# Kernel tuning notes

Hardware: AMD Instinct MI355X
Metric: run time of the kernel (lower is better)

## Reference

```python
import jax, jax.numpy as jnp
import numpy as np

N_EXPERT_CAPACITY = 2  # init kwarg; k = S * capacity // E


def setup_inputs() -> dict:
    key = jax.random.key(0)
    k1, k2, k3, k4 = jax.random.split(key, 4)
    B, S, D, E, F = 8, 1024, 1024, 8, 2048
    # kaiming-uniform-ish scales
    x = jax.random.normal(k1, (B, S, D), dtype=jnp.float32)
    choice_w = jax.random.uniform(k2, (E, D), dtype=jnp.float32, minval=-1.0, maxval=1.0) * (1.0 / np.sqrt(D))
    w1 = jax.random.uniform(k3, (E, D, F), dtype=jnp.float32, minval=-1.0, maxval=1.0) * (1.0 / np.sqrt(D))
    w2 = jax.random.uniform(k4, (E, F, D), dtype=jnp.float32, minval=-1.0, maxval=1.0) * (1.0 / np.sqrt(F))
    return {"x": x, "choice_w": choice_w, "w1": w1, "w2": w2}


def reference(x, choice_w, w1, w2):
    B, S, D = x.shape
    E = choice_w.shape[0]
    k = S * N_EXPERT_CAPACITY // E  # tokens per expert (expert-choice)
    # router softmax over experts: [B, S, E]
    probs = jax.nn.softmax(jnp.einsum('bsd,ed->bse', x, choice_w), axis=-1)
    # each expert picks its top-k tokens: G, I are [B, E, k]
    G, I = jax.lax.top_k(jnp.swapaxes(probs, -1, -2), k)
    # dispatch: gather tokens instead of one-hot matmul (same math)
    x_in = jnp.take_along_axis(x[:, None, :, :], I[..., None], axis=2)  # [B, E, k, D]
    # per-expert MLP with SiLU
    h = jax.nn.silu(jnp.einsum('bekd,edf->bekf', x_in, w1))  # [B, E, k, F]
    x_mlp = jnp.einsum('bekf,efd->bekd', h, w2)              # [B, E, k, D]
    # combine: weighted scatter-add back to token positions (equals P,G,x_mlp einsum)
    b_idx = jnp.arange(B)[:, None, None]  # [B,1,1] broadcasts with I [B,E,k]
    out = jnp.zeros_like(x).at[b_idx, I].add(G[..., None] * x_mlp)
    return out
```

## Files before the change

### kernel.cpp

```cpp
#include <hip/hip_runtime.h>
#include <hip/hip_bf16.h>
#include <math.h>

#define B_   8
#define S_   1024
#define D_   1024
#define E_   8
#define F_   2048
#define KCAP 256

typedef __bf16 bf16x8 __attribute__((ext_vector_type(8)));
typedef float  floatx4 __attribute__((ext_vector_type(4)));
typedef unsigned short ushortx8 __attribute__((ext_vector_type(8)));

__device__ __forceinline__ unsigned short f2b(float f) {
    union { float f; unsigned int u; } v; v.f = f;
    unsigned int u = v.u;
    u += 0x7fffu + ((u >> 16) & 1u);
    return (unsigned short)(u >> 16);
}
__device__ __forceinline__ float b2f(unsigned short u) {
    union { unsigned int u; float f; } v; v.u = ((unsigned)u) << 16; return v.f;
}

__device__ __forceinline__ void gl_lds16(const void* g, void* l) {
    __builtin_amdgcn_global_load_lds(
        (const __attribute__((address_space(1))) void*)g,
        (__attribute__((address_space(3))) void*)l, 16, 0, 0);
}

__device__ __forceinline__ unsigned long long topk_key(float p, int s) {
    return (((unsigned long long)__float_as_uint(p)) << 10) | (unsigned)(S_ - 1 - s);
}

#define PREP_DECODE(T, INP, OUTP, RV, CV, C0, R0) do { \
    int t_ = (T); \
    if (t_ < 4096) { \
        int e_ = t_ >> 9, tt_ = t_ & 511; \
        INP = w1 + (size_t)e_ * D_ * F_;  OUTP = w1t + (size_t)e_ * D_ * F_; \
        RV = D_; CV = F_; C0 = (tt_ & 63) * 32; R0 = (tt_ >> 6) * 128; \
    } else { \
        int t2_ = t_ - 4096; \
        int e_ = t2_ >> 9, tt_ = t2_ & 511; \
        INP = w2 + (size_t)e_ * D_ * F_;  OUTP = w2t + (size_t)e_ * D_ * F_; \
        RV = F_; CV = D_; C0 = (tt_ & 31) * 32; R0 = (tt_ >> 5) * 128; \
    } \
} while (0)

__device__ __forceinline__ void transpose_persist(
    const float* __restrict__ w1, const float* __restrict__ w2,
    unsigned short* __restrict__ w1t, unsigned short* __restrict__ w2t,
    float (*tile)[128][33], int T0, int Tend, int stride, int tid)
{
    const int lrow = tid >> 3;
    const int seg  = tid & 7;
    const int c    = tid >> 3;
    const int k    = tid & 7;

    const float* inp; unsigned short* outp; int R, C, c0, r0;
    PREP_DECODE(T0, inp, outp, R, C, c0, r0);
    float4 v[4];
#pragma unroll
    for (int i = 0; i < 4; i++)
        v[i] = *(const float4*)(inp + (size_t)(r0 + lrow + i * 32) * C + c0 + seg * 4);

    int buf = 0;
    for (int T = T0; T < Tend; T += stride) {
        unsigned short* oute = outp;
        const int Rr = R, cc0 = c0, rr0 = r0;
#pragma unroll
        for (int i = 0; i < 4; i++) {
            const int rr = lrow + i * 32;
            tile[buf][rr][seg * 4 + 0] = v[i].x;
            tile[buf][rr][seg * 4 + 1] = v[i].y;
            tile[buf][rr][seg * 4 + 2] = v[i].z;
            tile[buf][rr][seg * 4 + 3] = v[i].w;
        }
        if (T + stride < Tend) {
            PREP_DECODE(T + stride, inp, outp, R, C, c0, r0);
#pragma unroll
            for (int i = 0; i < 4; i++)
                v[i] = *(const float4*)(inp + (size_t)(r0 + lrow + i * 32) * C + c0 + seg * 4);
        }
        __builtin_amdgcn_sched_barrier(0);
        asm volatile("s_waitcnt lgkmcnt(0)" ::: "memory");
        __builtin_amdgcn_s_barrier();
        __builtin_amdgcn_sched_barrier(0);
#pragma unroll
        for (int srep = 0; srep < 2; srep++) {
            const int s8 = k + srep * 8;
            ushortx8 o;
#pragma unroll
            for (int j = 0; j < 8; j++) o[j] = f2b(tile[buf][s8 * 8 + j][c]);
            *(ushortx8*)(oute + (size_t)(cc0 + c) * Rr + rr0 + s8 * 8) = o;
        }
        buf ^= 1;
    }
}

__global__ void router_w1t_kernel(const float* __restrict__ x, const float* __restrict__ cw,
                                  float* __restrict__ probs, unsigned short* __restrict__ xb,
                                  const float* __restrict__ w1, const float* __restrict__ w2,
                                  unsigned short* __restrict__ w1t, unsigned short* __restrict__ w2t) {
    const int bid = blockIdx.x;
    const int tid = threadIdx.x;
    __shared__ float tile[2][128][33];

    if (bid < 384) {
        transpose_persist(w1, w2, w1t, w2t, tile, bid, 4096, 384, tid);
        return;
    }

    int gid  = (bid - 384) * 256 + tid;
    int wave = gid >> 6;
    int lane = gid & 63;
    int b = wave >> 10;
    int s = wave & (S_ - 1);
    const float* xrow = x + ((size_t)b * S_ + s) * D_;
    unsigned short* xbrow = xb + ((size_t)b * S_ + s) * D_;
    float acc[E_];
#pragma unroll
    for (int e = 0; e < E_; e++) acc[e] = 0.f;
#pragma unroll
    for (int it = 0; it < D_ / 256; it++) {
        int i = it * 256 + lane * 4;
        float4 xv = *(const float4*)(xrow + i);
        ushort4 o;
        o.x = f2b(xv.x); o.y = f2b(xv.y); o.z = f2b(xv.z); o.w = f2b(xv.w);
        *(ushort4*)(xbrow + i) = o;
#pragma unroll
        for (int e = 0; e < E_; e++) {
            float4 wv = *(const float4*)(cw + e * D_ + i);
            acc[e] = fmaf(xv.x, wv.x, fmaf(xv.y, wv.y, fmaf(xv.z, wv.z, fmaf(xv.w, wv.w, acc[e]))));
        }
    }
#pragma unroll
    for (int e = 0; e < E_; e++) {
        float v = acc[e];
#pragma unroll
        for (int off = 32; off >= 1; off >>= 1) v += __shfl_down(v, off, 64);
        acc[e] = v;
    }
    if (lane == 0) {
        float m = acc[0];
#pragma unroll
        for (int e = 1; e < E_; e++) m = fmaxf(m, acc[e]);
        float sum = 0.f;
#pragma unroll
        for (int e = 0; e < E_; e++) { acc[e] = __expf(acc[e] - m); sum += acc[e]; }
        float inv = 1.f / sum;
#pragma unroll
        for (int e = 0; e < E_; e++) probs[((size_t)b * E_ + e) * S_ + s] = acc[e] * inv;
    }
}

__global__ void topk_kernel(const float* __restrict__ probs, int* __restrict__ I,
                            float* __restrict__ G, unsigned short* __restrict__ Pmap) {
    const int be = blockIdx.x;
    const int b = be >> 3, e = be & 7;
    const int tid = threadIdx.x;
    __shared__ unsigned long long keys[S_];
    const float* rowp = probs + (size_t)be * S_;
#pragma unroll
    for (int q = 0; q < 4; q++) {
        const int s = q * 256 + tid;
        keys[s] = topk_key(rowp[s], s);
        Pmap[((size_t)(b * S_ + s)) * E_ + e] = 0;
    }
    __syncthreads();
    unsigned long long my[4];
    int r[4] = {0, 0, 0, 0};
#pragma unroll
    for (int q = 0; q < 4; q++) my[q] = keys[q * 256 + tid];
#pragma unroll 8
    for (int t = 0; t < S_; t++) {
        const unsigned long long kt = keys[t];
#pragma unroll
        for (int q = 0; q < 4; q++) r[q] += (kt > my[q]);
    }
#pragma unroll
    for (int q = 0; q < 4; q++) {
        if (r[q] < KCAP) {
            const int s = q * 256 + tid;
            I[be * KCAP + r[q]] = s;
            G[be * KCAP + r[q]] = rowp[s];
            Pmap[((size_t)(b * S_ + s)) * E_ + e] = (unsigned short)(r[q] + 1);
        }
    }
}


union GemmTransSm {
    struct {
        unsigned short Asm[128 * 64];
        unsigned short Bsm[128 * 64];
        unsigned int   ArowS[128];
    } g;
    float tile[2][128][33];
};

__global__ __launch_bounds__(256, 4) void gemm1_w2t_kernel(
    const unsigned short* __restrict__ xb,
    const unsigned short* __restrict__ w1t_,
    const int* __restrict__ I,
    unsigned short* __restrict__ H,
    const float* __restrict__ w1, const float* __restrict__ w2,
    unsigned short* __restrict__ w1t, unsigned short* __restrict__ w2t)
{
    __shared__ __align__(16) GemmTransSm sm;
    const int g   = blockIdx.x;
    const int tid = threadIdx.x;

    if (g >= 2048) {
        transpose_persist(w1, w2, w1t, w2t, sm.tile, 4096 + (g - 2048), 8192, 384, tid);
        return;
    }

    const int e  = g & 7;
    const int rr = g >> 3;
    const int b  = rr >> 5;
    const int t5 = rr & 31;
    const int be = b * 8 + e;
    const int mt = t5 & 1;
    const int nt = t5 >> 1;

    if (tid < 128) {
        int tok = I[(size_t)be * KCAP + mt * 128 + tid];
        sm.g.ArowS[tid] = (unsigned)((b * S_ + tok) * D_);
    }
    __syncthreads();

    const int r8   = tid >> 3;
    const int kseg = (tid & 7) ^ (r8 & 7);
    unsigned aoffW[4];
#pragma unroll
    for (int w = 0; w < 4; w++) aoffW[w] = sm.g.ArowS[w * 32 + r8] + kseg * 8;
    const size_t boff0 = ((size_t)e * F_ + nt * 128 + r8) * D_ + kseg * 8;

    const int lane = tid & 63;
    const int wv   = tid >> 6;
    const int wm   = (wv & 1) * 64;
    const int wn   = (wv >> 1) * 64;
    const int l15  = lane & 15;
    const int quad = lane >> 4;
    const int x0   = (quad ^ (l15 & 7)) * 8;

    int aoffs[4], boffs[4];
#pragma unroll
    for (int i = 0; i < 4; i++) {
        aoffs[i] = (wm + i * 16 + l15) * 64 + x0;
        boffs[i] = (wn + i * 16 + l15) * 64 + x0;
    }

    floatx4 acc[4][4];
#pragma unroll
    for (int i = 0; i < 4; i++)
#pragma unroll
        for (int j = 0; j < 4; j++) acc[i][j] = (floatx4){0.f, 0.f, 0.f, 0.f};

    for (int k0 = 0; k0 < D_; k0 += 64) {
#pragma unroll
        for (int w = 0; w < 4; w++) {
            gl_lds16(xb   + aoffW[w] + k0,                    &sm.g.Asm[(w * 256 + tid) * 8]);
            gl_lds16(w1t_ + boff0 + (size_t)w * 32 * D_ + k0, &sm.g.Bsm[(w * 256 + tid) * 8]);
        }
        __syncthreads();
        bf16x8 af[4], bfr[4];
#pragma unroll
        for (int i = 0; i < 4; i++) {
            af[i]  = *(const bf16x8*)&sm.g.Asm[aoffs[i]];
            bfr[i] = *(const bf16x8*)&sm.g.Bsm[boffs[i]];
        }
#pragma unroll
        for (int i = 0; i < 4; i++)
#pragma unroll
            for (int j = 0; j < 4; j++)
                acc[i][j] = __builtin_amdgcn_mfma_f32_16x16x32_bf16(af[i], bfr[j], acc[i][j], 0, 0, 0);
#pragma unroll
        for (int i = 0; i < 4; i++) {
            af[i]  = *(const bf16x8*)&sm.g.Asm[aoffs[i] ^ 32];
            bfr[i] = *(const bf16x8*)&sm.g.Bsm[boffs[i] ^ 32];
        }
#pragma unroll
        for (int i = 0; i < 4; i++)
#pragma unroll
            for (int j = 0; j < 4; j++)
                acc[i][j] = __builtin_amdgcn_mfma_f32_16x16x32_bf16(af[i], bfr[j], acc[i][j], 0, 0, 0);
        __syncthreads();
    }

    unsigned short* Hbe = H + (size_t)be * KCAP * F_;
#pragma unroll
    for (int i = 0; i < 4; i++) {
#pragma unroll
        for (int r = 0; r < 4; r++) {
            int m = mt * 128 + wm + i * 16 + quad * 4 + r;
            unsigned short* hrow = Hbe + (size_t)m * F_ + nt * 128;
#pragma unroll
            for (int j = 0; j < 4; j++) {
                float v = acc[i][j][r];
                float sv = v / (1.f + __expf(-v));
                hrow[wn + j * 16 + l15] = f2b(sv);
            }
        }
    }
}

__global__ __launch_bounds__(256, 4) void gemm2_kernel(
    const unsigned short* __restrict__ H,
    const unsigned short* __restrict__ w2t,
    unsigned short* __restrict__ xmlp)
{
    const int g  = blockIdx.x;
    const int e  = g & 7;
    const int rr = g >> 3;
    const int b  = rr >> 4;
    const int t4 = rr & 15;
    const int be = b * 8 + e;
    const int mt = t4 & 1;
    const int nt = t4 >> 1;
    const int tid = threadIdx.x;

    __shared__ __align__(16) unsigned short Asm2[128 * 64];
    __shared__ __align__(16) unsigned short Bsm2[128 * 64];

    const int r8   = tid >> 3;
    const int kseg = (tid & 7) ^ (r8 & 7);
    const size_t aoff0 = ((size_t)be * KCAP + mt * 128 + r8) * F_ + kseg * 8;
    const size_t boff0 = ((size_t)e * D_ + nt * 128 + r8) * F_ + kseg * 8;

    const int lane = tid & 63;
    const int wv   = tid >> 6;
    const int wm   = (wv & 1) * 64;
    const int wn   = (wv >> 1) * 64;
    const int l15  = lane & 15;
    const int quad = lane >> 4;
    const int x0   = (quad ^ (l15 & 7)) * 8;

    int aoffs[4], boffs[4];
#pragma unroll
    for (int i = 0; i < 4; i++) {
        aoffs[i] = (wm + i * 16 + l15) * 64 + x0;
        boffs[i] = (wn + i * 16 + l15) * 64 + x0;
    }

    floatx4 acc[4][4];
#pragma unroll
    for (int i = 0; i < 4; i++)
#pragma unroll
        for (int j = 0; j < 4; j++) acc[i][j] = (floatx4){0.f, 0.f, 0.f, 0.f};

    for (int k0 = 0; k0 < F_; k0 += 64) {
#pragma unroll
        for (int w = 0; w < 4; w++) {
            gl_lds16(H   + aoff0 + (size_t)w * 32 * F_ + k0, &Asm2[(w * 256 + tid) * 8]);
            gl_lds16(w2t + boff0 + (size_t)w * 32 * F_ + k0, &Bsm2[(w * 256 + tid) * 8]);
        }
        __syncthreads();
        bf16x8 af[4], bfr[4];
#pragma unroll
        for (int i = 0; i < 4; i++) {
            af[i]  = *(const bf16x8*)&Asm2[aoffs[i]];
            bfr[i] = *(const bf16x8*)&Bsm2[boffs[i]];
        }
#pragma unroll
        for (int i = 0; i < 4; i++)
#pragma unroll
            for (int j = 0; j < 4; j++)
                acc[i][j] = __builtin_amdgcn_mfma_f32_16x16x32_bf16(af[i], bfr[j], acc[i][j], 0, 0, 0);
#pragma unroll
        for (int i = 0; i < 4; i++) {
            af[i]  = *(const bf16x8*)&Asm2[aoffs[i] ^ 32];
            bfr[i] = *(const bf16x8*)&Bsm2[boffs[i] ^ 32];
        }
#pragma unroll
        for (int i = 0; i < 4; i++)
#pragma unroll
            for (int j = 0; j < 4; j++)
                acc[i][j] = __builtin_amdgcn_mfma_f32_16x16x32_bf16(af[i], bfr[j], acc[i][j], 0, 0, 0);
        __syncthreads();
    }

    unsigned short* Xbe = xmlp + (size_t)be * KCAP * D_;
#pragma unroll
    for (int i = 0; i < 4; i++) {
#pragma unroll
        for (int r = 0; r < 4; r++) {
            int m = mt * 128 + wm + i * 16 + quad * 4 + r;
            unsigned short* orow = Xbe + (size_t)m * D_ + nt * 128;
#pragma unroll
            for (int j = 0; j < 4; j++)
                orow[wn + j * 16 + l15] = f2b(acc[i][j][r]);
        }
    }
}

__global__ void combine_kernel(const unsigned short* __restrict__ xmlp,
                               const unsigned short* __restrict__ Pmap,
                               const float* __restrict__ G,
                               float* __restrict__ out) {
    int gid  = blockIdx.x * 256 + threadIdx.x;
    int wave = gid >> 6;
    int lane = gid & 63;
    int b = wave >> 10;
    float acc[16];
#pragma unroll
    for (int i = 0; i < 16; i++) acc[i] = 0.f;
    const unsigned short* pm = Pmap + (size_t)wave * E_;
#pragma unroll
    for (int e = 0; e < E_; e++) {
        int pe = pm[e];
        if (pe) {
            int beslot = (b * E_ + e) * KCAP + (pe - 1);
            float g = G[beslot];
            const unsigned short* rw = xmlp + (size_t)beslot * D_ + lane * 16;
            ushortx8 r0 = *(const ushortx8*)(rw);
            ushortx8 r1 = *(const ushortx8*)(rw + 8);
#pragma unroll
            for (int i = 0; i < 8; i++) {
                acc[i]     = fmaf(g, b2f(r0[i]), acc[i]);
                acc[8 + i] = fmaf(g, b2f(r1[i]), acc[8 + i]);
            }
        }
    }
    float* orow = out + (size_t)wave * D_ + lane * 16;
    ((float4*)orow)[0] = make_float4(acc[0],  acc[1],  acc[2],  acc[3]);
    ((float4*)orow)[1] = make_float4(acc[4],  acc[5],  acc[6],  acc[7]);
    ((float4*)orow)[2] = make_float4(acc[8],  acc[9],  acc[10], acc[11]);
    ((float4*)orow)[3] = make_float4(acc[12], acc[13], acc[14], acc[15]);
}

extern "C" void kernel_launch(void* const* d_in, const int* in_sizes, int n_in,
                              void* d_out, int out_size, void* d_ws, size_t ws_size,
                              hipStream_t stream) {
    const float* x  = (const float*)d_in[0];
    const float* cw = (const float*)d_in[1];
    const float* w1 = (const float*)d_in[2];
    const float* w2 = (const float*)d_in[3];
    float* out = (float*)d_out;

    char* ws = (char*)d_ws;
    float*          probs = (float*)(ws);
    int*            Ibuf  = (int*)(ws + 262144);
    float*          Gbuf  = (float*)(ws + 327680);
    unsigned short* Pmap  = (unsigned short*)(ws + 393216);
    unsigned short* xb    = (unsigned short*)(ws + 524288);
    unsigned short* w1t   = (unsigned short*)(ws + 17301504);
    unsigned short* xmlp  = w1t;
    unsigned short* w2t   = (unsigned short*)(ws + 50855936);
    unsigned short* Hbuf  = (unsigned short*)(ws + 84410368);

    router_w1t_kernel<<<384 + (B_ * S_ * 64) / 256, 256, 0, stream>>>(
        x, cw, probs, xb, w1, w2, w1t, w2t);
    topk_kernel<<<B_ * E_, 256, 0, stream>>>(probs, Ibuf, Gbuf, Pmap);
    gemm1_w2t_kernel<<<2048 + 384, 256, 0, stream>>>(
        xb, w1t, Ibuf, Hbuf, w1, w2, w1t, w2t);
    gemm2_kernel<<<B_ * E_ * 2 * (D_ / 128), 256, 0, stream>>>(Hbuf, w2t, xmlp);
    combine_kernel<<<(B_ * S_ * 64) / 256, 256, 0, stream>>>(xmlp, Pmap, Gbuf, out);
}
```

Measured before the change: 374.0 us.

## Move all weight transposes into the prep kernel and drop them from gemm1

Previously the w1/w2 bf16 transpose was split: 384 persistent blocks in the router kernel covered the first half of the tiles, and 384 extra blocks appended to gemm1 covered the second half (the w2 part) concurrently with the GEMM. Now the router/prep kernel launches 1024 transpose blocks that handle all 8192 tiles, and gemm1 becomes a pure GEMM with its own non-unioned shared memory. This gives up overlapping the w2 transpose with gemm1 compute in exchange for a simpler gemm1 and more transpose parallelism up front, risking a longer critical path in the first kernel.

```diff
diff --git a/kernel.cpp b/kernel.cpp
--- a/kernel.cpp
+++ b/kernel.cpp
@@ -98,20 +98,20 @@
     }
 }
 
-__global__ void router_w1t_kernel(const float* __restrict__ x, const float* __restrict__ cw,
-                                  float* __restrict__ probs, unsigned short* __restrict__ xb,
-                                  const float* __restrict__ w1, const float* __restrict__ w2,
-                                  unsigned short* __restrict__ w1t, unsigned short* __restrict__ w2t) {
+__global__ void prep_router_kernel(const float* __restrict__ x, const float* __restrict__ cw,
+                                   float* __restrict__ probs, unsigned short* __restrict__ xb,
+                                   const float* __restrict__ w1, const float* __restrict__ w2,
+                                   unsigned short* __restrict__ w1t, unsigned short* __restrict__ w2t) {
     const int bid = blockIdx.x;
     const int tid = threadIdx.x;
     __shared__ float tile[2][128][33];
 
-    if (bid < 384) {
-        transpose_persist(w1, w2, w1t, w2t, tile, bid, 4096, 384, tid);
+    if (bid < 1024) {
+        transpose_persist(w1, w2, w1t, w2t, tile, bid, 8192, 1024, tid);
         return;
     }
 
-    int gid  = (bid - 384) * 256 + tid;
+    int gid  = (bid - 1024) * 256 + tid;
     int wave = gid >> 6;
     int lane = gid & 63;
     int b = wave >> 10;
@@ -190,32 +190,13 @@
 }
 
 
-union GemmTransSm {
-    struct {
-        unsigned short Asm[128 * 64];
-        unsigned short Bsm[128 * 64];
-        unsigned int   ArowS[128];
-    } g;
-    float tile[2][128][33];
-};
-
-__global__ __launch_bounds__(256, 4) void gemm1_w2t_kernel(
+__global__ __launch_bounds__(256, 4) void gemm1_kernel(
     const unsigned short* __restrict__ xb,
-    const unsigned short* __restrict__ w1t_,
+    const unsigned short* __restrict__ w1t,
     const int* __restrict__ I,
-    unsigned short* __restrict__ H,
-    const float* __restrict__ w1, const float* __restrict__ w2,
-    unsigned short* __restrict__ w1t, unsigned short* __restrict__ w2t)
+    unsigned short* __restrict__ H)
 {
-    __shared__ __align__(16) GemmTransSm sm;
-    const int g   = blockIdx.x;
-    const int tid = threadIdx.x;
-
-    if (g >= 2048) {
-        transpose_persist(w1, w2, w1t, w2t, sm.tile, 4096 + (g - 2048), 8192, 384, tid);
-        return;
-    }
-
+    const int g  = blockIdx.x;
     const int e  = g & 7;
     const int rr = g >> 3;
     const int b  = rr >> 5;
@@ -223,10 +204,15 @@
     const int be = b * 8 + e;
     const int mt = t5 & 1;
     const int nt = t5 >> 1;
+    const int tid = threadIdx.x;
+
+    __shared__ __align__(16) unsigned short Asm[128 * 64];
+    __shared__ __align__(16) unsigned short Bsm[128 * 64];
+    __shared__ unsigned int ArowS[128];
 
     if (tid < 128) {
         int tok = I[(size_t)be * KCAP + mt * 128 + tid];
-        sm.g.ArowS[tid] = (unsigned)((b * S_ + tok) * D_);
+        ArowS[tid] = (unsigned)((b * S_ + tok) * D_);
     }
     __syncthreads();
 
@@ -234,7 +220,7 @@
     const int kseg = (tid & 7) ^ (r8 & 7);
     unsigned aoffW[4];
 #pragma unroll
-    for (int w = 0; w < 4; w++) aoffW[w] = sm.g.ArowS[w * 32 + r8] + kseg * 8;
+    for (int w = 0; w < 4; w++) aoffW[w] = ArowS[w * 32 + r8] + kseg * 8;
     const size_t boff0 = ((size_t)e * F_ + nt * 128 + r8) * D_ + kseg * 8;
 
     const int lane = tid & 63;
@@ -261,15 +247,15 @@
     for (int k0 = 0; k0 < D_; k0 += 64) {
 #pragma unroll
         for (int w = 0; w < 4; w++) {
-            gl_lds16(xb   + aoffW[w] + k0,                    &sm.g.Asm[(w * 256 + tid) * 8]);
-            gl_lds16(w1t_ + boff0 + (size_t)w * 32 * D_ + k0, &sm.g.Bsm[(w * 256 + tid) * 8]);
+            gl_lds16(xb  + aoffW[w] + k0,                    &Asm[(w * 256 + tid) * 8]);
+            gl_lds16(w1t + boff0 + (size_t)w * 32 * D_ + k0, &Bsm[(w * 256 + tid) * 8]);
         }
         __syncthreads();
         bf16x8 af[4], bfr[4];
 #pragma unroll
         for (int i = 0; i < 4; i++) {
-            af[i]  = *(const bf16x8*)&sm.g.Asm[aoffs[i]];
-            bfr[i] = *(const bf16x8*)&sm.g.Bsm[boffs[i]];
+            af[i]  = *(const bf16x8*)&Asm[aoffs[i]];
+            bfr[i] = *(const bf16x8*)&Bsm[boffs[i]];
         }
 #pragma unroll
         for (int i = 0; i < 4; i++)
@@ -278,8 +264,8 @@
                 acc[i][j] = __builtin_amdgcn_mfma_f32_16x16x32_bf16(af[i], bfr[j], acc[i][j], 0, 0, 0);
 #pragma unroll
         for (int i = 0; i < 4; i++) {
-            af[i]  = *(const bf16x8*)&sm.g.Asm[aoffs[i] ^ 32];
-            bfr[i] = *(const bf16x8*)&sm.g.Bsm[boffs[i] ^ 32];
+            af[i]  = *(const bf16x8*)&Asm[aoffs[i] ^ 32];
+            bfr[i] = *(const bf16x8*)&Bsm[boffs[i] ^ 32];
         }
 #pragma unroll
         for (int i = 0; i < 4; i++)
@@ -450,11 +436,10 @@
     unsigned short* w2t   = (unsigned short*)(ws + 50855936);
     unsigned short* Hbuf  = (unsigned short*)(ws + 84410368);
 
-    router_w1t_kernel<<<384 + (B_ * S_ * 64) / 256, 256, 0, stream>>>(
+    prep_router_kernel<<<1024 + (B_ * S_ * 64) / 256, 256, 0, stream>>>(
         x, cw, probs, xb, w1, w2, w1t, w2t);
     topk_kernel<<<B_ * E_, 256, 0, stream>>>(probs, Ibuf, Gbuf, Pmap);
-    gemm1_w2t_kernel<<<2048 + 384, 256, 0, stream>>>(
-        xb, w1t, Ibuf, Hbuf, w1, w2, w1t, w2t);
+    gemm1_kernel<<<B_ * E_ * 2 * (F_ / 128), 256, 0, stream>>>(xb, w1t, Ibuf, Hbuf);
     gemm2_kernel<<<B_ * E_ * 2 * (D_ / 128), 256, 0, stream>>>(Hbuf, w2t, xmlp);
     combine_kernel<<<(B_ * S_ * 64) / 256, 256, 0, stream>>>(xmlp, Pmap, Gbuf, out);
 }
```

Result: no change. 377.1 us (+0.8%).
